# Kernel tuning notes

Hardware: AMD Instinct MI355X
Metric: run time of the kernel (lower is better)

The kernel has to match this reference:

```python
import jax, jax.numpy as jnp
import numpy as np

N_NODES = 50000
N_EDGES = 500000
D = 128
BN_EPS = 1e-5


def setup_inputs() -> dict:
    key = jax.random.key(0)
    ks = jax.random.split(key, 6)
    x = jax.random.normal(ks[0], (N_NODES, D), dtype=jnp.float32)
    edge_attr = jax.random.normal(ks[1], (N_EDGES, D), dtype=jnp.float32)
    edge_source = jax.random.randint(ks[2], (N_EDGES,), 0, N_NODES, dtype=jnp.int32)
    edge_target = jax.random.randint(ks[3], (N_EDGES,), 0, N_NODES, dtype=jnp.int32)
    # Linear weights stored as [in, out] = [3*D, D]; scaled like torch default init
    scale = 1.0 / np.sqrt(3 * D)
    Wf = jax.random.normal(ks[4], (3 * D, D), dtype=jnp.float32) * scale
    Ws = jax.random.normal(ks[5], (3 * D, D), dtype=jnp.float32) * scale
    bf = jnp.zeros((D,), dtype=jnp.float32)
    bs = jnp.zeros((D,), dtype=jnp.float32)
    gamma = jnp.ones((D,), dtype=jnp.float32)
    beta = jnp.zeros((D,), dtype=jnp.float32)
    return {"x": x, "edge_attr": edge_attr, "edge_source": edge_source,
            "edge_target": edge_target, "Wf": Wf, "bf": bf, "Ws": Ws, "bs": bs,
            "gamma": gamma, "beta": beta}


def reference(x, edge_attr, edge_source, edge_target, Wf, bf, Ws, bs, gamma, beta):
    # gather + concat: z is [E, 3*D]
    z = jnp.concatenate([x[edge_source], x[edge_target], edge_attr], axis=-1)
    # gated edge messages: sigmoid(linear_f(z)) * softplus(linear_s(z))  [E, D]
    msg = jax.nn.sigmoid(z @ Wf + bf) * jax.nn.softplus(z @ Ws + bs)
    # scatter-sum back to source nodes  [N, D]
    agg = jax.ops.segment_sum(msg, edge_source, num_segments=N_NODES)
    # BatchNorm1d (training mode: batch stats, biased variance)
    mean = jnp.mean(agg, axis=0)
    var = jnp.var(agg, axis=0)
    agg_bn = (agg - mean) * jax.lax.rsqrt(var + BN_EPS) * gamma + beta
    return jax.nn.softplus(x + agg_bn)
```

## Files before the change

kernel.cpp:

```cpp
#include <hip/hip_runtime.h>
#include <math.h>
#include <stdint.h>

#define N_NODES 50000
#define N_EDGES 500000
#define D 128
#define BE 64
#define NKT 6
#define WROW 72
#define WSLAB (256 * WROW)
#define LOG2E 1.4426950408889634f
#define LN2   0.6931471805599453f

typedef __attribute__((ext_vector_type(8))) short bf16x8;
typedef __attribute__((ext_vector_type(4))) float floatx4;

__device__ __forceinline__ float fast_sigmoid(float v) {
    return __builtin_amdgcn_rcpf(1.0f + __builtin_amdgcn_exp2f(-v * LOG2E));
}
__device__ __forceinline__ float fast_softplus(float v) {
    float t = __builtin_amdgcn_exp2f(-fabsf(v) * LOG2E);
    return fmaxf(v, 0.0f) + __builtin_amdgcn_logf(1.0f + t) * LN2;
}
__device__ __forceinline__ uint32_t pack_bf16(float a, float b) {
    union { float f; uint32_t u; } ca, cb; ca.f = a; cb.f = b;
    return __builtin_amdgcn_perm(cb.u + 0x8000u, ca.u + 0x8000u, 0x07060302);
}
__device__ __forceinline__ unsigned short f2bf(float f) {
    union { float f; uint32_t u; } c; c.f = f;
    return (unsigned short)((c.u + 0x8000u) >> 16);
}

__global__ __launch_bounds__(256) void wt_prepass(
    const float* __restrict__ Wf, const float* __restrict__ Ws,
    unsigned short* __restrict__ Wt)
{
    const int kt = blockIdx.x >> 3;
    const int i  = blockIdx.x & 7;
    const int n  = threadIdx.x;
    const float* src = (n < 128) ? (Wf + n) : (Ws + (n - 128));
    const int k0 = kt * 64 + i * 8;
    uint32_t u[4];
#pragma unroll
    for (int j = 0; j < 4; j++) {
        float a = src[(size_t)(k0 + 2 * j) * D];
        float b = src[(size_t)(k0 + 2 * j + 1) * D];
        u[j] = pack_bf16(a, b);
    }
    uint4 v; v.x = u[0]; v.y = u[1]; v.z = u[2]; v.w = u[3];
    *(uint4*)(Wt + (size_t)(kt * 256 + n) * WROW + i * 8) = v;
}

__global__ __launch_bounds__(256) void edge_msg_mfma(
    const float* __restrict__ x, const float* __restrict__ edge_attr,
    const int* __restrict__ esrc, const int* __restrict__ etgt,
    const unsigned short* __restrict__ Wt,
    const float* __restrict__ bfp, const float* __restrict__ bsp,
    float* __restrict__ agg, unsigned short* __restrict__ msgs, int mode)
{
    __shared__ unsigned short sW[WSLAB];
    __shared__ unsigned short sZ[BE * WROW];
    __shared__ int sSrc[BE];
    __shared__ int sTgt[BE];

    const int tid  = threadIdx.x;
    const int lane = tid & 63;
    const int w    = tid >> 6;
    const int e0   = blockIdx.x * BE;

    if (tid < BE) {
        sSrc[tid] = (e0 + tid < N_EDGES) ? esrc[e0 + tid] : 0;
    } else if (tid < 2 * BE) {
        int m = tid - BE;
        sTgt[m] = (e0 + m < N_EDGES) ? etgt[e0 + m] : 0;
    }
    __syncthreads();

    floatx4 acc[4][4];
#pragma unroll
    for (int mt = 0; mt < 4; mt++)
#pragma unroll
        for (int nt = 0; nt < 4; nt++) {
            floatx4 z = {0.f, 0.f, 0.f, 0.f};
            acc[mt][nt] = z;
        }

    const int zm = tid >> 2;
    const int zk = (tid & 3) * 16;

#pragma unroll 1
    for (int kt = 0; kt < NKT; kt++) {
        {
            const char* gbase = (const char*)Wt + (size_t)kt * 36864 + w * 9216 + lane * 16;
            char* lbase = (char*)sW + w * 9216;
#pragma unroll
            for (int i = 0; i < 9; i++) {
                __builtin_amdgcn_global_load_lds(
                    (const __attribute__((address_space(1))) void*)(gbase + i * 1024),
                    (__attribute__((address_space(3))) void*)(lbase + i * 1024),
                    16, 0, 0);
            }
        }
        {
            const float* zsrc;
            int half = (kt & 1) * 64;
            if (kt < 2)      zsrc = x + (size_t)sSrc[zm] * D + half;
            else if (kt < 4) zsrc = x + (size_t)sTgt[zm] * D + half;
            else {
                int eg = e0 + zm;
                zsrc = edge_attr + (size_t)(eg < N_EDGES ? eg : 0) * D + half;
            }
            float4 f0 = *(const float4*)(zsrc + zk);
            float4 f1 = *(const float4*)(zsrc + zk + 4);
            float4 f2 = *(const float4*)(zsrc + zk + 8);
            float4 f3 = *(const float4*)(zsrc + zk + 12);
            uint4 lo, hi;
            lo.x = pack_bf16(f0.x, f0.y); lo.y = pack_bf16(f0.z, f0.w);
            lo.z = pack_bf16(f1.x, f1.y); lo.w = pack_bf16(f1.z, f1.w);
            hi.x = pack_bf16(f2.x, f2.y); hi.y = pack_bf16(f2.z, f2.w);
            hi.z = pack_bf16(f3.x, f3.y); hi.w = pack_bf16(f3.z, f3.w);
            uint32_t* dz = (uint32_t*)(sZ + (size_t)zm * WROW) + (zk >> 1);
            *(uint4*)(dz)     = lo;
            *(uint4*)(dz + 4) = hi;
        }
        __syncthreads();

#pragma unroll
        for (int ks = 0; ks < 2; ks++) {
            const int kb = ks * 32 + (lane >> 4) * 8;
            bf16x8 afr[4];
#pragma unroll
            for (int mt = 0; mt < 4; mt++)
                afr[mt] = *(const bf16x8*)(sZ + (mt * 16 + (lane & 15)) * WROW + kb);
            bf16x8 bfr[4];
#pragma unroll
            for (int nt = 0; nt < 4; nt++) {
                int n = (nt < 2) ? (w * 32 + nt * 16 + (lane & 15))
                                 : (128 + w * 32 + (nt - 2) * 16 + (lane & 15));
                bfr[nt] = *(const bf16x8*)(sW + n * WROW + kb);
            }
#pragma unroll
            for (int mt = 0; mt < 4; mt++)
#pragma unroll
                for (int nt = 0; nt < 4; nt++)
                    acc[mt][nt] = __builtin_amdgcn_mfma_f32_16x16x32_bf16(
                        afr[mt], bfr[nt], acc[mt][nt], 0, 0, 0);
        }
        __syncthreads();
    }

#pragma unroll
    for (int nt = 0; nt < 2; nt++) {
        const int col = w * 32 + nt * 16 + (lane & 15);
        const float bF = bfp[col];
        const float bS = bsp[col];
#pragma unroll
        for (int mt = 0; mt < 4; mt++) {
#pragma unroll
            for (int r = 0; r < 4; r++) {
                int mm = mt * 16 + (lane >> 4) * 4 + r;
                int eg = e0 + mm;
                if (eg >= N_EDGES) continue;
                float f = acc[mt][nt][r] + bF;
                float s = acc[mt][nt + 2][r] + bS;
                float msg = fast_sigmoid(f) * fast_softplus(s);
                if (mode) {
                    msgs[(size_t)eg * D + col] = f2bf(msg);
                } else {
                    atomicAdd(agg + (size_t)sSrc[mm] * D + col, msg);
                }
            }
        }
    }
}

__global__ __launch_bounds__(512) void count_kernel(
    const int* __restrict__ esrc, int* __restrict__ cnt)
{
    int e = blockIdx.x * 512 + threadIdx.x;
    if (e < N_EDGES) atomicAdd(&cnt[esrc[e]], 1);
}

__global__ __launch_bounds__(1024) void scan_kernel(
    const int* __restrict__ cnt, int* __restrict__ ofs)
{
    __shared__ int part[1024];
    const int t = threadIdx.x;
    const int CH = (N_NODES + 1023) / 1024;
    const int i0 = t * CH;
    int s = 0;
    for (int j = 0; j < CH; j++) {
        int i = i0 + j;
        if (i < N_NODES) s += cnt[i];
    }
    part[t] = s;
    __syncthreads();
    for (int off = 1; off < 1024; off <<= 1) {
        int v = (t >= off) ? part[t - off] : 0;
        __syncthreads();
        part[t] += v;
        __syncthreads();
    }
    int running = part[t] - s;
    for (int j = 0; j < CH; j++) {
        int i = i0 + j;
        if (i < N_NODES) { ofs[i] = running; running += cnt[i]; }
    }
}

__global__ __launch_bounds__(512) void fill_kernel(
    const int* __restrict__ esrc, int* __restrict__ ofs, int* __restrict__ eidx)
{
    int e = blockIdx.x * 512 + threadIdx.x;
    if (e < N_EDGES) {
        int slot = atomicAdd(&ofs[esrc[e]], 1);
        eidx[slot] = e;
    }
}

__global__ __launch_bounds__(512) void gather_kernel(
    const unsigned short* __restrict__ msgs, const int* __restrict__ eidx,
    const int* __restrict__ cnt, const int* __restrict__ ofs,
    float* __restrict__ agg)
{
    const int lane = threadIdx.x & 63;
    const int w    = threadIdx.x >> 6;
    const int n    = blockIdx.x * 8 + w;
    if (n >= N_NODES) return;
    const int deg  = cnt[n];
    const int base = ofs[n] - deg;
    float a0 = 0.0f, a1 = 0.0f;
    for (int j = 0; j < deg; j++) {
        int id = eidx[base + j];
        uint32_t p = *(const uint32_t*)(msgs + (size_t)id * D + 2 * lane);
        union { uint32_t u; float f; } c0, c1;
        c0.u = p << 16;
        c1.u = p & 0xFFFF0000u;
        a0 += c0.f; a1 += c1.f;
    }
    float2 o; o.x = a0; o.y = a1;
    *(float2*)(agg + (size_t)n * D + 2 * lane) = o;
}

#define STATS_BLOCKS 128
__global__ __launch_bounds__(256) void bn_stats_kernel(
    const float* __restrict__ agg, float* __restrict__ stats)
{
    __shared__ float4 redS[256];
    __shared__ float4 redQ[256];
    const int c4 = threadIdx.x & 31;
    const int rg = threadIdx.x >> 5;
    const int rows = (N_NODES + STATS_BLOCKS - 1) / STATS_BLOCKS;
    const int r0 = blockIdx.x * rows;
    const int r1 = min(r0 + rows, N_NODES);
    const float4* a4 = (const float4*)agg;

    float4 s = {0, 0, 0, 0}, q = {0, 0, 0, 0};
    for (int r = r0 + rg; r < r1; r += 8) {
        float4 v = a4[(size_t)r * 32 + c4];
        s.x += v.x; s.y += v.y; s.z += v.z; s.w += v.w;
        q.x += v.x * v.x; q.y += v.y * v.y; q.z += v.z * v.z; q.w += v.w * v.w;
    }
    redS[threadIdx.x] = s;
    redQ[threadIdx.x] = q;
    __syncthreads();
    if (rg == 0) {
#pragma unroll
        for (int j = 1; j < 8; j++) {
            float4 ts = redS[c4 + j * 32], tq = redQ[c4 + j * 32];
            s.x += ts.x; s.y += ts.y; s.z += ts.z; s.w += ts.w;
            q.x += tq.x; q.y += tq.y; q.z += tq.z; q.w += tq.w;
        }
        atomicAdd(&stats[c4 * 4 + 0], s.x);
        atomicAdd(&stats[c4 * 4 + 1], s.y);
        atomicAdd(&stats[c4 * 4 + 2], s.z);
        atomicAdd(&stats[c4 * 4 + 3], s.w);
        atomicAdd(&stats[D + c4 * 4 + 0], q.x);
        atomicAdd(&stats[D + c4 * 4 + 1], q.y);
        atomicAdd(&stats[D + c4 * 4 + 2], q.z);
        atomicAdd(&stats[D + c4 * 4 + 3], q.w);
    }
}

__global__ __launch_bounds__(256) void bn_final_kernel(
    const float* __restrict__ x, const float* __restrict__ agg,
    const float* __restrict__ stats,
    const float* __restrict__ gamma, const float* __restrict__ beta,
    float* __restrict__ out)
{
    const int idx = blockIdx.x * blockDim.x + threadIdx.x;
    const int total4 = N_NODES * D / 4;
    if (idx >= total4) return;
    const int c4 = idx & (D / 4 - 1);
    const float inv_n = 1.0f / (float)N_NODES;

    float4 sm = *(const float4*)&stats[c4 * 4];
    float4 sq = *(const float4*)&stats[D + c4 * 4];
    float4 g  = *(const float4*)&gamma[c4 * 4];
    float4 b  = *(const float4*)&beta[c4 * 4];
    float4 xv = ((const float4*)x)[idx];
    float4 av = ((const float4*)agg)[idx];

    float4 o;
    {
        float mean = sm.x * inv_n, var = sq.x * inv_n - mean * mean;
        float is = rsqrtf(var + 1e-5f) * g.x;
        o.x = fast_softplus(xv.x + (av.x - mean) * is + b.x);
    }
    {
        float mean = sm.y * inv_n, var = sq.y * inv_n - mean * mean;
        float is = rsqrtf(var + 1e-5f) * g.y;
        o.y = fast_softplus(xv.y + (av.y - mean) * is + b.y);
    }
    {
        float mean = sm.z * inv_n, var = sq.z * inv_n - mean * mean;
        float is = rsqrtf(var + 1e-5f) * g.z;
        o.z = fast_softplus(xv.z + (av.z - mean) * is + b.z);
    }
    {
        float mean = sm.w * inv_n, var = sq.w * inv_n - mean * mean;
        float is = rsqrtf(var + 1e-5f) * g.w;
        o.w = fast_softplus(xv.w + (av.w - mean) * is + b.w);
    }
    ((float4*)out)[idx] = o;
}

extern "C" void kernel_launch(void* const* d_in, const int* in_sizes, int n_in,
                              void* d_out, int out_size, void* d_ws, size_t ws_size,
                              hipStream_t stream) {
    const float* x         = (const float*)d_in[0];
    const float* edge_attr = (const float*)d_in[1];
    const int*   esrc      = (const int*)d_in[2];
    const int*   etgt      = (const int*)d_in[3];
    const float* Wf        = (const float*)d_in[4];
    const float* bf_       = (const float*)d_in[5];
    const float* Ws        = (const float*)d_in[6];
    const float* bs_       = (const float*)d_in[7];
    const float* gamma     = (const float*)d_in[8];
    const float* beta      = (const float*)d_in[9];
    float* out = (float*)d_out;

    float* agg   = (float*)d_ws;
    float* stats = agg + (size_t)N_NODES * D;
    int*   cnt   = (int*)(stats + 2 * D);
    int*   ofs   = cnt + N_NODES;
    unsigned short* Wt = (unsigned short*)(ofs + N_NODES);
    int*   eidx  = (int*)((char*)Wt + 221184);
    unsigned short* msgs = (unsigned short*)(eidx + N_EDGES);
    const size_t NEED = 25600000ULL + 1024 + 400000 + 221184 + 2000000 + 128000000ULL;
    const int mode = (ws_size >= NEED) ? 1 : 0;

    wt_prepass<<<48, 256, 0, stream>>>(Wf, Ws, Wt);
    if (mode) {
        hipMemsetAsync(stats, 0, 1024 + 200000, stream);
        edge_msg_mfma<<<(N_EDGES + BE - 1) / BE, 256, 0, stream>>>(
            x, edge_attr, esrc, etgt, Wt, bf_, bs_, agg, msgs, 1);
        count_kernel<<<(N_EDGES + 511) / 512, 512, 0, stream>>>(esrc, cnt);
        scan_kernel<<<1, 1024, 0, stream>>>(cnt, ofs);
        fill_kernel<<<(N_EDGES + 511) / 512, 512, 0, stream>>>(esrc, ofs, eidx);
        gather_kernel<<<(N_NODES + 7) / 8, 512, 0, stream>>>(msgs, eidx, cnt, ofs, agg);
    } else {
        hipMemsetAsync(d_ws, 0, ((size_t)N_NODES * D + 2 * D) * sizeof(float), stream);
        edge_msg_mfma<<<(N_EDGES + BE - 1) / BE, 256, 0, stream>>>(
            x, edge_attr, esrc, etgt, Wt, bf_, bs_, agg, msgs, 0);
    }
    bn_stats_kernel<<<STATS_BLOCKS, 256, 0, stream>>>(agg, stats);
    bn_final_kernel<<<(N_NODES * D / 4 + 255) / 256, 256, 0, stream>>>(
        x, agg, stats, gamma, beta, out);
}
```

Before: 784.3 us.

## Stage bf16 messages via LDS for coalesced stores, fuse degree count, parallelize scan

The edge kernel now writes bf16 messages into shared memory (reusing the weight slab) and then emits coalesced 16-byte row stores, replacing the previous scattered 2-byte stores. It also performs the per-source degree count itself, so the separate count kernel is removed. The single-block scan becomes a two-level scan, with block offsets added in the fill and gather kernels. The gather kernel splits each node's edges across two wavefronts and combines them through shared memory. These changes add an extra barrier and some LDS traffic in the edge kernel, plus one more small kernel launch.

```diff
diff --git a/kernel.cpp b/kernel.cpp
--- a/kernel.cpp
+++ b/kernel.cpp
@@ -9,6 +9,7 @@
 #define NKT 6
 #define WROW 72
 #define WSLAB (256 * WROW)
+#define MROW 136
 #define LOG2E 1.4426950408889634f
 #define LN2   0.6931471805599453f
 
@@ -56,7 +57,8 @@
     const int* __restrict__ esrc, const int* __restrict__ etgt,
     const unsigned short* __restrict__ Wt,
     const float* __restrict__ bfp, const float* __restrict__ bsp,
-    float* __restrict__ agg, unsigned short* __restrict__ msgs, int mode)
+    float* __restrict__ agg, unsigned short* __restrict__ msgs,
+    int* __restrict__ cnt, int mode)
 {
     __shared__ unsigned short sW[WSLAB];
     __shared__ unsigned short sZ[BE * WROW];
@@ -149,88 +151,117 @@
         __syncthreads();
     }
 
-#pragma unroll
-    for (int nt = 0; nt < 2; nt++) {
-        const int col = w * 32 + nt * 16 + (lane & 15);
-        const float bF = bfp[col];
-        const float bS = bsp[col];
-#pragma unroll
-        for (int mt = 0; mt < 4; mt++) {
-#pragma unroll
-            for (int r = 0; r < 4; r++) {
-                int mm = mt * 16 + (lane >> 4) * 4 + r;
-                int eg = e0 + mm;
-                if (eg >= N_EDGES) continue;
-                float f = acc[mt][nt][r] + bF;
-                float s = acc[mt][nt + 2][r] + bS;
-                float msg = fast_sigmoid(f) * fast_softplus(s);
-                if (mode) {
-                    msgs[(size_t)eg * D + col] = f2bf(msg);
-                } else {
-                    atomicAdd(agg + (size_t)sSrc[mm] * D + col, msg);
+    if (mode) {
+        unsigned short* sM = sW;
+#pragma unroll
+        for (int nt = 0; nt < 2; nt++) {
+            const int col = w * 32 + nt * 16 + (lane & 15);
+            const float bF = bfp[col];
+            const float bS = bsp[col];
+#pragma unroll
+            for (int mt = 0; mt < 4; mt++) {
+#pragma unroll
+                for (int r = 0; r < 4; r++) {
+                    int mm = mt * 16 + (lane >> 4) * 4 + r;
+                    float f = acc[mt][nt][r] + bF;
+                    float s = acc[mt][nt + 2][r] + bS;
+                    sM[mm * MROW + col] = f2bf(fast_sigmoid(f) * fast_softplus(s));
                 }
             }
         }
-    }
-}
-
-__global__ __launch_bounds__(512) void count_kernel(
-    const int* __restrict__ esrc, int* __restrict__ cnt)
-{
-    int e = blockIdx.x * 512 + threadIdx.x;
-    if (e < N_EDGES) atomicAdd(&cnt[esrc[e]], 1);
-}
-
-__global__ __launch_bounds__(1024) void scan_kernel(
-    const int* __restrict__ cnt, int* __restrict__ ofs)
-{
-    __shared__ int part[1024];
+        __syncthreads();
+        {
+            const int r = tid >> 2;
+            const int c = tid & 3;
+            if (e0 + r < N_EDGES) {
+                const uint4* sp = (const uint4*)(sM + r * MROW + c * 32);
+                uint4 v0 = sp[0], v1 = sp[1], v2 = sp[2], v3 = sp[3];
+                uint4* dp = (uint4*)(msgs + (size_t)(e0 + r) * D + c * 32);
+                dp[0] = v0; dp[1] = v1; dp[2] = v2; dp[3] = v3;
+            }
+        }
+        if (tid < BE && e0 + tid < N_EDGES) atomicAdd(&cnt[sSrc[tid]], 1);
+    } else {
+#pragma unroll
+        for (int nt = 0; nt < 2; nt++) {
+            const int col = w * 32 + nt * 16 + (lane & 15);
+            const float bF = bfp[col];
+            const float bS = bsp[col];
+#pragma unroll
+            for (int mt = 0; mt < 4; mt++) {
+#pragma unroll
+                for (int r = 0; r < 4; r++) {
+                    int mm = mt * 16 + (lane >> 4) * 4 + r;
+                    int eg = e0 + mm;
+                    if (eg >= N_EDGES) continue;
+                    float f = acc[mt][nt][r] + bF;
+                    float s = acc[mt][nt + 2][r] + bS;
+                    atomicAdd(agg + (size_t)sSrc[mm] * D + col,
+                              fast_sigmoid(f) * fast_softplus(s));
+                }
+            }
+        }
+    }
+}
+
+__global__ __launch_bounds__(1024) void scan1_kernel(
+    const int* __restrict__ cnt, int* __restrict__ ofs, int* __restrict__ bsum)
+{
+    __shared__ int sh[1024];
     const int t = threadIdx.x;
-    const int CH = (N_NODES + 1023) / 1024;
-    const int i0 = t * CH;
-    int s = 0;
-    for (int j = 0; j < CH; j++) {
-        int i = i0 + j;
-        if (i < N_NODES) s += cnt[i];
-    }
-    part[t] = s;
+    const int n = blockIdx.x * 1024 + t;
+    int c = (n < N_NODES) ? cnt[n] : 0;
+    sh[t] = c;
     __syncthreads();
     for (int off = 1; off < 1024; off <<= 1) {
-        int v = (t >= off) ? part[t - off] : 0;
+        int v = (t >= off) ? sh[t - off] : 0;
         __syncthreads();
-        part[t] += v;
+        sh[t] += v;
         __syncthreads();
     }
-    int running = part[t] - s;
-    for (int j = 0; j < CH; j++) {
-        int i = i0 + j;
-        if (i < N_NODES) { ofs[i] = running; running += cnt[i]; }
+    if (n < N_NODES) ofs[n] = sh[t] - c;
+    if (t == 1023) bsum[blockIdx.x] = sh[1023];
+}
+
+__global__ __launch_bounds__(64) void scan2_kernel(int* __restrict__ bsum)
+{
+    if (threadIdx.x == 0) {
+        int v[49];
+#pragma unroll
+        for (int i = 0; i < 49; i++) v[i] = bsum[i];
+        int run = 0;
+#pragma unroll
+        for (int i = 0; i < 49; i++) { bsum[i] = run; run += v[i]; }
     }
 }
 
 __global__ __launch_bounds__(512) void fill_kernel(
-    const int* __restrict__ esrc, int* __restrict__ ofs, int* __restrict__ eidx)
+    const int* __restrict__ esrc, int* __restrict__ ofs,
+    const int* __restrict__ bsum, int* __restrict__ eidx)
 {
     int e = blockIdx.x * 512 + threadIdx.x;
     if (e < N_EDGES) {
-        int slot = atomicAdd(&ofs[esrc[e]], 1);
+        int s = esrc[e];
+        int slot = atomicAdd(&ofs[s], 1) + bsum[s >> 10];
         eidx[slot] = e;
     }
 }
 
-__global__ __launch_bounds__(512) void gather_kernel(
+__global__ __launch_bounds__(256) void gather_kernel(
     const unsigned short* __restrict__ msgs, const int* __restrict__ eidx,
     const int* __restrict__ cnt, const int* __restrict__ ofs,
-    float* __restrict__ agg)
-{
-    const int lane = threadIdx.x & 63;
-    const int w    = threadIdx.x >> 6;
-    const int n    = blockIdx.x * 8 + w;
-    if (n >= N_NODES) return;
+    const int* __restrict__ bsum, float* __restrict__ agg)
+{
+    __shared__ float red[2][64][2];
+    const int tid  = threadIdx.x;
+    const int lane = tid & 63;
+    const int w2   = (tid >> 6) & 1;
+    const int h    = tid >> 7;
+    const int n    = blockIdx.x * 2 + h;
     const int deg  = cnt[n];
-    const int base = ofs[n] - deg;
+    const int base = bsum[n >> 10] + ofs[n] - deg;
     float a0 = 0.0f, a1 = 0.0f;
-    for (int j = 0; j < deg; j++) {
+    for (int j = w2; j < deg; j += 2) {
         int id = eidx[base + j];
         uint32_t p = *(const uint32_t*)(msgs + (size_t)id * D + 2 * lane);
         union { uint32_t u; float f; } c0, c1;
@@ -238,8 +269,14 @@
         c1.u = p & 0xFFFF0000u;
         a0 += c0.f; a1 += c1.f;
     }
-    float2 o; o.x = a0; o.y = a1;
-    *(float2*)(agg + (size_t)n * D + 2 * lane) = o;
+    if (w2 == 1) { red[h][lane][0] = a0; red[h][lane][1] = a1; }
+    __syncthreads();
+    if (w2 == 0) {
+        a0 += red[h][lane][0];
+        a1 += red[h][lane][1];
+        float2 o; o.x = a0; o.y = a1;
+        *(float2*)(agg + (size_t)n * D + 2 * lane) = o;
+    }
 }
 
 #define STATS_BLOCKS 128
@@ -344,25 +381,27 @@
     float* stats = agg + (size_t)N_NODES * D;
     int*   cnt   = (int*)(stats + 2 * D);
     int*   ofs   = cnt + N_NODES;
-    unsigned short* Wt = (unsigned short*)(ofs + N_NODES);
+    int*   bsum  = ofs + N_NODES;
+    unsigned short* Wt = (unsigned short*)(bsum + 256);
     int*   eidx  = (int*)((char*)Wt + 221184);
     unsigned short* msgs = (unsigned short*)(eidx + N_EDGES);
-    const size_t NEED = 25600000ULL + 1024 + 400000 + 221184 + 2000000 + 128000000ULL;
+    const size_t NEED = 25600000ULL + 1024 + 200000 + 200000 + 1024
+                      + 221184 + 2000000 + 128000000ULL;
     const int mode = (ws_size >= NEED) ? 1 : 0;
 
     wt_prepass<<<48, 256, 0, stream>>>(Wf, Ws, Wt);
     if (mode) {
         hipMemsetAsync(stats, 0, 1024 + 200000, stream);
         edge_msg_mfma<<<(N_EDGES + BE - 1) / BE, 256, 0, stream>>>(
-            x, edge_attr, esrc, etgt, Wt, bf_, bs_, agg, msgs, 1);
-        count_kernel<<<(N_EDGES + 511) / 512, 512, 0, stream>>>(esrc, cnt);
-        scan_kernel<<<1, 1024, 0, stream>>>(cnt, ofs);
-        fill_kernel<<<(N_EDGES + 511) / 512, 512, 0, stream>>>(esrc, ofs, eidx);
-        gather_kernel<<<(N_NODES + 7) / 8, 512, 0, stream>>>(msgs, eidx, cnt, ofs, agg);
+            x, edge_attr, esrc, etgt, Wt, bf_, bs_, agg, msgs, cnt, 1);
+        scan1_kernel<<<49, 1024, 0, stream>>>(cnt, ofs, bsum);
+        scan2_kernel<<<1, 64, 0, stream>>>(bsum);
+        fill_kernel<<<(N_EDGES + 511) / 512, 512, 0, stream>>>(esrc, ofs, bsum, eidx);
+        gather_kernel<<<N_NODES / 2, 256, 0, stream>>>(msgs, eidx, cnt, ofs, bsum, agg);
     } else {
         hipMemsetAsync(d_ws, 0, ((size_t)N_NODES * D + 2 * D) * sizeof(float), stream);
         edge_msg_mfma<<<(N_EDGES + BE - 1) / BE, 256, 0, stream>>>(
-            x, edge_attr, esrc, etgt, Wt, bf_, bs_, agg, msgs, 0);
+            x, edge_attr, esrc, etgt, Wt, bf_, bs_, agg, msgs, cnt, 0);
     }
     bn_stats_kernel<<<STATS_BLOCKS, 256, 0, stream>>>(agg, stats);
     bn_final_kernel<<<(N_NODES * D / 4 + 255) / 256, 256, 0, stream>>>(
```

Result: faster. 660.1 us (-15.8%).
